# Optimization experiments

Measured on AMD Instinct MI355X. Metric: run time of the kernel, lower is better.

The kernel has to match this reference:

```python
import jax, jax.numpy as jnp
import numpy as np

NUM_SITES_X = 2048
NUM_SITES_Y = 4096
NUM_CLB_SITES = 6_000_000
NUM_SLICE_SITES = 6_000_000
NUM_SITES = NUM_SITES_X * NUM_SITES_Y  # global flattened site-id space


def setup_inputs() -> dict:
    key = jax.random.key(0)
    k1, k2, k3, k4 = jax.random.split(key, 4)
    # CLB slice site ids (x*num_sites_y + y), sorted as produced from the column-major fabric scan
    slice_sites = jnp.sort(
        jax.random.randint(k1, (NUM_SLICE_SITES,), 0, NUM_SITES, dtype=jnp.int32))
    # per-CLB-site signature count; >0 means the site already has instances committed
    site_det_sig_idx = jax.random.randint(
        k2, (NUM_CLB_SITES,), 0, 4, dtype=jnp.int32)
    # compact CLB address -> global site id map (monotone by construction in the original)
    addr2site_map = jnp.sort(
        jax.random.randint(k3, (NUM_CLB_SITES,), 0, NUM_SITES, dtype=jnp.int32))
    # per-slice-site legalization score (site_det_score analogue)
    site_scores = jax.random.normal(k4, (NUM_SLICE_SITES,), dtype=jnp.float32)
    return {
        "slice_sites": slice_sites,
        "site_det_sig_idx": site_det_sig_idx,
        "addr2site_map": addr2site_map,
        "site_scores": site_scores,
    }


def _remaining_mask(slice_sites, site_det_sig_idx, addr2site_map):
    """Faithful jit-friendly version of compute_remaining_slice_sites.

    torch/np original:
      assigned = addr2site_map[site_det_sig_idx > 0]
      mask[np.in1d(slice_sites, assigned)] = True; return ~mask
    We avoid the data-dependent boolean gather by replacing unassigned
    entries with a -1 sentinel (site ids are >= 0), sorting, and doing a
    vectorized membership test via searchsorted.
    """
    n = addr2site_map.shape[0]
    assigned = jnp.where(site_det_sig_idx > 0, addr2site_map, jnp.int32(-1))
    assigned_sorted = jnp.sort(assigned)  # sentinels land at the front
    pos = jnp.searchsorted(assigned_sorted, slice_sites, side="left")
    pos = jnp.clip(pos, 0, n - 1)
    found = assigned_sorted[pos] == slice_sites  # in1d membership
    return ~found  # True where the slice site is still available


def reference(slice_sites, site_det_sig_idx, addr2site_map, site_scores):
    remaining = _remaining_mask(slice_sites, site_det_sig_idx, addr2site_map)
    # scores of still-available candidate sites (zeros where already assigned)
    avail_scores = jnp.where(remaining, site_scores, jnp.zeros((), site_scores.dtype))
    return remaining, avail_scores
```

## Files before the change

kernel.cpp:

```cpp
#include <hip/hip_runtime.h>


typedef int   v4i __attribute__((ext_vector_type(4)));
typedef float v4f __attribute__((ext_vector_type(4)));

static constexpr int NUM_SITES_TOTAL = 2048 * 4096;
static constexpr int WORDS_PER_BLOCK = 128;
static constexpr int SITES_PER_BLOCK = WORDS_PER_BLOCK * 32;
static constexpr int GRID            = NUM_SITES_TOTAL / SITES_PER_BLOCK;
static constexpr int BLOCK           = 256;
static constexpr int CHUNK           = 16;

__global__ __launch_bounds__(BLOCK) void fused_kernel(
    const int*   __restrict__ ss,
    const int*   __restrict__ sig,
    const int*   __restrict__ a2s,
    const float* __restrict__ sc,
    float*       __restrict__ rem,
    float*       __restrict__ avail,
    int n_slice, int n_clb)
{
    __shared__ unsigned int lbm[WORDS_PER_BLOCK];

    const int siteBase = blockIdx.x * SITES_PER_BLOCK;
    const int siteEnd  = siteBase + SITES_PER_BLOCK;

    for (int w = threadIdx.x; w < WORDS_PER_BLOCK; w += BLOCK) lbm[w] = 0u;

    int lo = 0, hi = n_clb;
    while (lo < hi) { int m = (lo + hi) >> 1; if (a2s[m] < siteBase) lo = m + 1; else hi = m; }
    const int e0 = lo;
    hi = n_clb;
    while (lo < hi) { int m = (lo + hi) >> 1; if (a2s[m] < siteEnd) lo = m + 1; else hi = m; }
    const int e1 = lo;

    lo = 0; hi = n_slice;
    while (lo < hi) { int m = (lo + hi) >> 1; if (ss[m] < siteBase) lo = m + 1; else hi = m; }
    const int p0 = lo;
    hi = n_slice;
    while (lo < hi) { int m = (lo + hi) >> 1; if (ss[m] < siteEnd) lo = m + 1; else hi = m; }
    const int p1 = lo;

    __syncthreads();

    const int start = e0 & ~(CHUNK - 1);
    for (int s = start + threadIdx.x * CHUNK; s < e1; s += BLOCK * CHUNK) {
        int av[CHUNK], gv[CHUNK];
        if (s + CHUNK <= n_clb) {
            const v4i* ap = (const v4i*)(a2s + s);
            const v4i* gp = (const v4i*)(sig + s);
#pragma unroll
            for (int q = 0; q < CHUNK / 4; ++q) {
                v4i a = ap[q];
                av[4*q+0] = a.x; av[4*q+1] = a.y; av[4*q+2] = a.z; av[4*q+3] = a.w;
                v4i g = gp[q];
                gv[4*q+0] = g.x; gv[4*q+1] = g.y; gv[4*q+2] = g.z; gv[4*q+3] = g.w;
            }
        } else {
#pragma unroll
            for (int j = 0; j < CHUNK; ++j) {
                const int i = s + j;
                const bool ok = i < n_clb;
                av[j] = ok ? a2s[i] : -1;
                gv[j] = ok ? sig[i] : 0;
            }
        }

        unsigned int curw = 0xFFFFFFFFu, curm = 0u;
#pragma unroll
        for (int j = 0; j < CHUNK; ++j) {
            const int site = av[j];
            if (gv[j] > 0 && site >= siteBase && site < siteEnd) {
                const unsigned int u = (unsigned int)(site - siteBase);
                const unsigned int w = u >> 5;
                const unsigned int m = 1u << (u & 31u);
                if (w == curw) curm |= m;
                else { if (curm) atomicOr(&lbm[curw], curm); curw = w; curm = m; }
            }
        }
        if (curm) atomicOr(&lbm[curw], curm);
    }

    __syncthreads();

    int i0 = (p0 + 3) & ~3;
    int i1 = p1 & ~3;
    if (i1 < i0) i1 = i0;

    for (int q = (i0 >> 2) + threadIdx.x; q < (i1 >> 2); q += BLOCK) {
        v4i s = __builtin_nontemporal_load((const v4i*)ss + q);
        v4f f = __builtin_nontemporal_load((const v4f*)sc + q);
        v4f r, a;
#pragma unroll
        for (int j = 0; j < 4; ++j) {
            const unsigned int u   = (unsigned int)(s[j] - siteBase);
            const unsigned int bit = (lbm[u >> 5] >> (u & 31u)) & 1u;
            r[j] = bit ? 0.0f : 1.0f;
            a[j] = bit ? 0.0f : f[j];
        }
        __builtin_nontemporal_store(r, (v4f*)rem + q);
        __builtin_nontemporal_store(a, (v4f*)avail + q);
    }
    for (int i = p0 + threadIdx.x; i < min(i0, p1); i += BLOCK) {
        const unsigned int u   = (unsigned int)(ss[i] - siteBase);
        const unsigned int bit = (lbm[u >> 5] >> (u & 31u)) & 1u;
        rem[i]   = bit ? 0.0f : 1.0f;
        avail[i] = bit ? 0.0f : sc[i];
    }
    for (int i = max(i1, p0) + threadIdx.x; i < p1; i += BLOCK) {
        const unsigned int u   = (unsigned int)(ss[i] - siteBase);
        const unsigned int bit = (lbm[u >> 5] >> (u & 31u)) & 1u;
        rem[i]   = bit ? 0.0f : 1.0f;
        avail[i] = bit ? 0.0f : sc[i];
    }
}

extern "C" void kernel_launch(void* const* d_in, const int* in_sizes, int n_in,
                              void* d_out, int out_size, void* d_ws, size_t ws_size,
                              hipStream_t stream) {
    const int*   slice_sites = (const int*)d_in[0];
    const int*   sig         = (const int*)d_in[1];
    const int*   a2s         = (const int*)d_in[2];
    const float* scores      = (const float*)d_in[3];
    const int n_slice = in_sizes[0];
    const int n_clb   = in_sizes[1];

    float* rem   = (float*)d_out;
    float* avail = rem + n_slice;

    fused_kernel<<<GRID, BLOCK, 0, stream>>>(
        slice_sites, sig, a2s, scores, rem, avail, n_slice, n_clb);
}
```

Before: 160.4 us.

## Precompute per-block search boundaries in a separate kernel and shrink scatter chunk

```diff
diff --git a/kernel.cpp b/kernel.cpp
--- a/kernel.cpp
+++ b/kernel.cpp
@@ -9,66 +9,68 @@
 static constexpr int SITES_PER_BLOCK = WORDS_PER_BLOCK * 32;
 static constexpr int GRID            = NUM_SITES_TOTAL / SITES_PER_BLOCK;
 static constexpr int BLOCK           = 256;
-static constexpr int CHUNK           = 16;
+
+__global__ __launch_bounds__(BLOCK) void boundary_kernel(
+    const int* __restrict__ ss, const int* __restrict__ a2s,
+    int* __restrict__ eb, int* __restrict__ pb, int n_slice, int n_clb)
+{
+    const int g = blockIdx.x * BLOCK + threadIdx.x;
+    if (g > GRID) return;
+    const int key = g * SITES_PER_BLOCK;
+
+    int lo = 0, hi = n_clb;
+    while (lo < hi) { int m = (lo + hi) >> 1; if (a2s[m] < key) lo = m + 1; else hi = m; }
+    eb[g] = lo;
+
+    lo = 0; hi = n_slice;
+    while (lo < hi) { int m = (lo + hi) >> 1; if (ss[m] < key) lo = m + 1; else hi = m; }
+    pb[g] = lo;
+}
 
 __global__ __launch_bounds__(BLOCK) void fused_kernel(
     const int*   __restrict__ ss,
     const int*   __restrict__ sig,
     const int*   __restrict__ a2s,
     const float* __restrict__ sc,
+    const int*   __restrict__ eb,
+    const int*   __restrict__ pb,
     float*       __restrict__ rem,
     float*       __restrict__ avail,
-    int n_slice, int n_clb)
+    int n_clb)
 {
     __shared__ unsigned int lbm[WORDS_PER_BLOCK];
 
-    const int siteBase = blockIdx.x * SITES_PER_BLOCK;
+    const int g        = blockIdx.x;
+    const int siteBase = g * SITES_PER_BLOCK;
     const int siteEnd  = siteBase + SITES_PER_BLOCK;
 
     for (int w = threadIdx.x; w < WORDS_PER_BLOCK; w += BLOCK) lbm[w] = 0u;
 
-    int lo = 0, hi = n_clb;
-    while (lo < hi) { int m = (lo + hi) >> 1; if (a2s[m] < siteBase) lo = m + 1; else hi = m; }
-    const int e0 = lo;
-    hi = n_clb;
-    while (lo < hi) { int m = (lo + hi) >> 1; if (a2s[m] < siteEnd) lo = m + 1; else hi = m; }
-    const int e1 = lo;
-
-    lo = 0; hi = n_slice;
-    while (lo < hi) { int m = (lo + hi) >> 1; if (ss[m] < siteBase) lo = m + 1; else hi = m; }
-    const int p0 = lo;
-    hi = n_slice;
-    while (lo < hi) { int m = (lo + hi) >> 1; if (ss[m] < siteEnd) lo = m + 1; else hi = m; }
-    const int p1 = lo;
+    const int e0 = eb[g], e1 = eb[g + 1];
+    const int p0 = pb[g], p1 = pb[g + 1];
 
     __syncthreads();
 
-    const int start = e0 & ~(CHUNK - 1);
-    for (int s = start + threadIdx.x * CHUNK; s < e1; s += BLOCK * CHUNK) {
-        int av[CHUNK], gv[CHUNK];
-        if (s + CHUNK <= n_clb) {
-            const v4i* ap = (const v4i*)(a2s + s);
-            const v4i* gp = (const v4i*)(sig + s);
-#pragma unroll
-            for (int q = 0; q < CHUNK / 4; ++q) {
-                v4i a = ap[q];
-                av[4*q+0] = a.x; av[4*q+1] = a.y; av[4*q+2] = a.z; av[4*q+3] = a.w;
-                v4i g = gp[q];
-                gv[4*q+0] = g.x; gv[4*q+1] = g.y; gv[4*q+2] = g.z; gv[4*q+3] = g.w;
-            }
+    const int mstart = e0 & ~3;
+    for (int s = mstart + threadIdx.x * 4; s < e1; s += BLOCK * 4) {
+        int av[4], gv[4];
+        if (s + 4 <= n_clb) {
+            v4i a = __builtin_nontemporal_load((const v4i*)(a2s + s));
+            v4i gg = __builtin_nontemporal_load((const v4i*)(sig + s));
+            av[0]=a.x; av[1]=a.y; av[2]=a.z; av[3]=a.w;
+            gv[0]=gg.x; gv[1]=gg.y; gv[2]=gg.z; gv[3]=gg.w;
         } else {
 #pragma unroll
-            for (int j = 0; j < CHUNK; ++j) {
+            for (int j = 0; j < 4; ++j) {
                 const int i = s + j;
                 const bool ok = i < n_clb;
                 av[j] = ok ? a2s[i] : -1;
                 gv[j] = ok ? sig[i] : 0;
             }
         }
-
         unsigned int curw = 0xFFFFFFFFu, curm = 0u;
 #pragma unroll
-        for (int j = 0; j < CHUNK; ++j) {
+        for (int j = 0; j < 4; ++j) {
             const int site = av[j];
             if (gv[j] > 0 && site >= siteBase && site < siteEnd) {
                 const unsigned int u = (unsigned int)(site - siteBase);
@@ -125,9 +127,15 @@
     const int n_slice = in_sizes[0];
     const int n_clb   = in_sizes[1];
 
+    int* eb = (int*)d_ws;
+    int* pb = eb + (GRID + 1);
+
+    boundary_kernel<<<(GRID + 1 + BLOCK - 1) / BLOCK, BLOCK, 0, stream>>>(
+        slice_sites, a2s, eb, pb, n_slice, n_clb);
+
     float* rem   = (float*)d_out;
     float* avail = rem + n_slice;
 
     fused_kernel<<<GRID, BLOCK, 0, stream>>>(
-        slice_sites, sig, a2s, scores, rem, avail, n_slice, n_clb);
+        slice_sites, sig, a2s, scores, eb, pb, rem, avail, n_clb);
 }
```

New measurement: 157.5 us. Within noise of the previous version (-1.8%).
